# Performance work log

Measured on AMD Instinct MI355X. Metric: run time of the kernel, lower is better.

## Reference

```python
import jax, jax.numpy as jnp
import numpy as np

B, N, D = 4, 4096, 1024
STD = 1.0 / D

def setup_inputs() -> dict:
    key = jax.random.key(0)
    ks = jax.random.split(key, 6)
    return {
        "x_real": jax.random.normal(ks[0], (B, N, D), dtype=jnp.float32),
        "x_imag": jax.random.normal(ks[1], (B, N, D), dtype=jnp.float32),
        "w_query_real": jax.random.normal(ks[2], (D, D), dtype=jnp.float32) * STD,
        "w_query_imag": jax.random.normal(ks[3], (D, D), dtype=jnp.float32) * STD,
        "w_key": jax.random.normal(ks[4], (D, D), dtype=jnp.float32) * STD,
        "w_value": jax.random.normal(ks[5], (D, D), dtype=jnp.float32) * STD,
    }

def reference(x_real, x_imag, w_query_real, w_query_imag, w_key, w_value):
    # query gate: (x.real @ Wqr) * (x.imag @ Wqi)  -> [b, n, e]
    query = jnp.einsum('bnd,de->bne', x_real, w_query_real) * \
            jnp.einsum('bnd,de->bne', x_imag, w_query_imag)
    key = jnp.einsum('bnd,de->bne', x_real, w_key)      # [b, n, d]
    value = jnp.einsum('bnd,de->bne', x_imag, w_value)  # [b, n, e]
    # linear-attention style reduction over sequence dim n
    kv_attn = jnp.einsum('bnd,bne->bde', key, value)    # [b, d, e]
    # dropout with p=0.0 (eval / identity)
    bffn = jnp.einsum('bnd,bde->bne', query, kv_attn)   # [b, n, e]
    return bffn
```

## Files before the change

### kernel.cpp

```cpp
#include <hip/hip_runtime.h>
#include <stdint.h>

typedef unsigned short ushort_t;
typedef __attribute__((ext_vector_type(8))) short bf16x8;
typedef __attribute__((ext_vector_type(4))) float f32x4;

__device__ __forceinline__ ushort_t f2bf(float f) {
  union { float f; uint32_t u; } v; v.f = f;
  uint32_t u = v.u;
  u += 0x7FFFu + ((u >> 16) & 1u);
  return (ushort_t)(u >> 16);
}
__device__ __forceinline__ float bf2f(ushort_t h) {
  union { uint32_t u; float f; } v; v.u = ((uint32_t)h) << 16;
  return v.f;
}
__device__ __forceinline__ void gl2lds16(const void* g, void* l) {
  __builtin_amdgcn_global_load_lds(
      (__attribute__((address_space(1))) void*)(uintptr_t)g,
      (__attribute__((address_space(3))) void*)(uint32_t)(uintptr_t)l,
      16, 0, 0);
}


template <bool F32OUT>
__device__ __forceinline__ void gemm256x128(
    const ushort_t* __restrict__ A, int lda,
    const ushort_t* __restrict__ Bt, int ldb,
    int m0, int n0, int K, char* __restrict__ smem,
    f32x4 (&acc)[4][4]) {
  const int t = threadIdx.x;
  const int nt = K >> 5;
  const int rowS = t >> 2;
  const int kgS = (t & 3) ^ ((t >> 3) & 3);
  const ushort_t* a0 = A + (size_t)(m0 + rowS) * lda + kgS * 8;
  const ushort_t* a1 = a0 + (size_t)128 * lda;
  const ushort_t* b0 = Bt + (size_t)(n0 + rowS) * ldb + kgS * 8;
  const int d0 = t * 16;
  const int lane = t & 63, wid = t >> 6;
  const int wm = wid >> 1, wn = wid & 1;
  const int lr = lane & 15, lq = lane >> 4;
  const int o = lr * 64 + ((lq ^ ((lr >> 1) & 3)) << 4);
  const int aW = wm * 4096;
  const int bW = 16384 + wn * 4096;

#define STAGE(tt, buf) do { \
    char* s = smem + (buf); \
    gl2lds16(a0 + (tt) * 32, s + d0); \
    gl2lds16(a1 + (tt) * 32, s + 8192 + d0); \
    gl2lds16(b0 + (tt) * 32, s + 16384 + d0); \
  } while (0)

  bf16x8 aF[4], bF[4];
  STAGE(0, 0);
  for (int tt = 0; tt < nt; ++tt) {
    asm volatile("s_waitcnt vmcnt(0) lgkmcnt(0)\n\ts_barrier" ::: "memory");
    const int cb = (tt & 1) ? 24576 : 0;
    if (tt + 1 < nt) STAGE(tt + 1, (tt & 1) ? 0 : 24576);
    const char* base = smem + cb;
    #pragma unroll
    for (int mi = 0; mi < 4; ++mi)
      aF[mi] = *(const bf16x8*)(base + aW + mi * 1024 + o);
    #pragma unroll
    for (int ni = 0; ni < 4; ++ni)
      bF[ni] = *(const bf16x8*)(base + bW + ni * 1024 + o);
    __builtin_amdgcn_s_setprio(1);
    #pragma unroll
    for (int mi = 0; mi < 4; ++mi)
      #pragma unroll
      for (int ni = 0; ni < 4; ++ni)
        acc[mi][ni] = __builtin_amdgcn_mfma_f32_16x16x32_bf16(aF[mi], bF[ni], acc[mi][ni], 0, 0, 0);
    __builtin_amdgcn_s_setprio(0);
  }
#undef STAGE
}

__global__ __launch_bounds__(512, 2) void gq(
    const ushort_t* __restrict__ Xr, const ushort_t* __restrict__ Xi,
    const ushort_t* __restrict__ Wr, const ushort_t* __restrict__ Wi,
    ushort_t* __restrict__ Q) {
  extern __shared__ char smem[];
  const int bid = blockIdx.x;
  const int xcd = bid & 7, i = bid >> 3;
  const int m0 = (xcd * 8 + (i >> 3)) * 256;
  const int n0 = (i & 7) * 128;
  const int t = threadIdx.x;
  const int lane = t & 63, wid = t >> 6;
  const int wm = wid >> 1, wn = wid & 1;
  const int lr = lane & 15, lq = lane >> 4;

  const int rowS = t >> 2;
  const int kgS = (t & 3) ^ ((t >> 3) & 3);
  const ushort_t* ar0 = Xr + (size_t)(m0 + rowS) * 1024 + kgS * 8;
  const ushort_t* ar1 = ar0 + (size_t)128 * 1024;
  const ushort_t* ai0 = Xi + (size_t)(m0 + rowS) * 1024 + kgS * 8;
  const ushort_t* ai1 = ai0 + (size_t)128 * 1024;
  const ushort_t* br0 = Wr + (size_t)(n0 + rowS) * 1024 + kgS * 8;
  const ushort_t* bi0 = Wi + (size_t)(n0 + rowS) * 1024 + kgS * 8;
  const int d0 = t * 16;
  const int o = lr * 64 + ((lq ^ ((lr >> 1) & 3)) << 4);
  const int aW = wm * 4096;
  const int bW = wn * 4096;

#define STAGEQ(tt, buf) do { \
    char* s = smem + (buf); \
    gl2lds16(ar0 + (tt) * 32, s + d0); \
    gl2lds16(ar1 + (tt) * 32, s + 8192 + d0); \
    gl2lds16(ai0 + (tt) * 32, s + 16384 + d0); \
    gl2lds16(ai1 + (tt) * 32, s + 24576 + d0); \
    gl2lds16(br0 + (tt) * 32, s + 32768 + d0); \
    gl2lds16(bi0 + (tt) * 32, s + 40960 + d0); \
  } while (0)

  f32x4 accR[4][4] = {}, accI[4][4] = {};
  bf16x8 aR[4], aI[4], bR[4], bI[4];

  STAGEQ(0, 0);
  for (int tt = 0; tt < 32; ++tt) {
    asm volatile("s_waitcnt vmcnt(0) lgkmcnt(0)\n\ts_barrier" ::: "memory");
    const int cb = (tt & 1) ? 49152 : 0;
    if (tt + 1 < 32) STAGEQ(tt + 1, (tt & 1) ? 0 : 49152);
    const char* base = smem + cb;
    #pragma unroll
    for (int mi = 0; mi < 4; ++mi) {
      aR[mi] = *(const bf16x8*)(base + aW + mi * 1024 + o);
      aI[mi] = *(const bf16x8*)(base + 16384 + aW + mi * 1024 + o);
    }
    #pragma unroll
    for (int ni = 0; ni < 4; ++ni) {
      bR[ni] = *(const bf16x8*)(base + 32768 + bW + ni * 1024 + o);
      bI[ni] = *(const bf16x8*)(base + 40960 + bW + ni * 1024 + o);
    }
    __builtin_amdgcn_s_setprio(1);
    #pragma unroll
    for (int mi = 0; mi < 4; ++mi)
      #pragma unroll
      for (int ni = 0; ni < 4; ++ni) {
        accR[mi][ni] = __builtin_amdgcn_mfma_f32_16x16x32_bf16(aR[mi], bR[ni], accR[mi][ni], 0, 0, 0);
        accI[mi][ni] = __builtin_amdgcn_mfma_f32_16x16x32_bf16(aI[mi], bI[ni], accI[mi][ni], 0, 0, 0);
      }
    __builtin_amdgcn_s_setprio(0);
  }
#undef STAGEQ

  #pragma unroll
  for (int mi = 0; mi < 4; ++mi) {
    int rbase = m0 + wm * 64 + mi * 16 + lq * 4;
    #pragma unroll
    for (int ni = 0; ni < 4; ++ni) {
      int c = n0 + wn * 64 + ni * 16 + lr;
      #pragma unroll
      for (int r = 0; r < 4; ++r)
        Q[(size_t)(rbase + r) * 1024 + c] = f2bf(accR[mi][ni][r] * accI[mi][ni][r]);
    }
  }
}

__global__ __launch_bounds__(512, 4) void gpart(
    const ushort_t* __restrict__ XrT, const ushort_t* __restrict__ XiT,
    float* __restrict__ P) {
  extern __shared__ char smem[];
  const int bid = blockIdx.x;
  const int xcd = bid & 7, i = bid >> 3;
  const int z = xcd * 2 + (i >> 5);
  const int mn = i & 31;
  const int m0 = (mn >> 3) * 256, n0 = (mn & 7) * 128;
  const int b = z & 3, s = z >> 2;
  const ushort_t* A = XrT + ((size_t)b << 22) + s * 1024;
  const ushort_t* Bt = XiT + ((size_t)b << 22) + s * 1024;
  f32x4 acc[4][4] = {};
  gemm256x128<true>(A, 4096, Bt, 4096, m0, n0, 1024, smem, acc);

  const int t = threadIdx.x, lane = t & 63, wid = t >> 6;
  const int wm = wid >> 1, wn = wid & 1;
  const int lr = lane & 15, lq = lane >> 4;
  float* C = P + ((size_t)z << 20);
  #pragma unroll
  for (int mi = 0; mi < 4; ++mi) {
    int rbase = m0 + wm * 64 + mi * 16 + lq * 4;
    #pragma unroll
    for (int ni = 0; ni < 4; ++ni) {
      int c = n0 + wn * 64 + ni * 16 + lr;
      #pragma unroll
      for (int r = 0; r < 4; ++r)
        C[(size_t)(rbase + r) * 1024 + c] = acc[mi][ni][r];
    }
  }
}

__global__ __launch_bounds__(256) void g_reduce(const float* __restrict__ P,
                                                ushort_t* __restrict__ G) {
  size_t e4 = ((size_t)blockIdx.x * 256 + threadIdx.x) * 4;
  int b = (int)(e4 >> 20);
  size_t j = e4 & ((1u << 20) - 1);
  float s0 = 0.f, s1 = 0.f, s2 = 0.f, s3 = 0.f;
  #pragma unroll
  for (int sp = 0; sp < 4; ++sp) {
    float4 v = *(const float4*)(P + ((size_t)(sp * 4 + b) << 20) + j);
    s0 += v.x; s1 += v.y; s2 += v.z; s3 += v.w;
  }
  *(ushort4*)&G[e4] = make_ushort4(f2bf(s0), f2bf(s1), f2bf(s2), f2bf(s3));
}

__global__ __launch_bounds__(256, 4) void gemm1k(
    const ushort_t* __restrict__ Abase, int aStride,
    const ushort_t* __restrict__ Btbase, int btStride,
    ushort_t* __restrict__ Cbase) {
  extern __shared__ char smem[];
  const int bid = blockIdx.x;
  const int b = bid >> 6, mn = bid & 63;
  const int m0 = (mn >> 3) * 128, n0 = (mn & 7) * 128;
  const ushort_t* A = Abase + (size_t)b * (size_t)aStride;
  const ushort_t* Bt = Btbase + (size_t)b * (size_t)btStride;

  const int t = threadIdx.x;
  const int lane = t & 63, wid = t >> 6;
  const int wm = wid >> 1, wn = wid & 1;
  const int lr = lane & 15, lq = lane >> 4;
  const int rowS = t >> 2;
  const int kgS = (t & 3) ^ ((t >> 3) & 3);
  const ushort_t* a0 = A + (size_t)(m0 + rowS) * 1024 + kgS * 8;
  const ushort_t* a1 = a0 + (size_t)64 * 1024;
  const ushort_t* b0 = Bt + (size_t)(n0 + rowS) * 1024 + kgS * 8;
  const ushort_t* b1 = b0 + (size_t)64 * 1024;
  const int d0 = t * 16, d1 = 4096 + t * 16;
  const int o = lr * 64 + ((lq ^ ((lr >> 1) & 3)) << 4);
  const int aW = wm * 4096;
  const int bW = 8192 + wn * 4096;

#define STG1(tt, buf) do { \
    char* s = smem + (buf); \
    gl2lds16(a0 + (tt) * 32, s + d0); \
    gl2lds16(a1 + (tt) * 32, s + d1); \
    gl2lds16(b0 + (tt) * 32, s + 8192 + d0); \
    gl2lds16(b1 + (tt) * 32, s + 8192 + d1); \
  } while (0)

  f32x4 acc[4][4] = {};
  bf16x8 aF[4], bF[4];
  STG1(0, 0);
  for (int tt = 0; tt < 32; ++tt) {
    asm volatile("s_waitcnt vmcnt(0) lgkmcnt(0)\n\ts_barrier" ::: "memory");
    const int cb = (tt & 1) ? 16384 : 0;
    if (tt + 1 < 32) STG1(tt + 1, (tt & 1) ? 0 : 16384);
    const char* base = smem + cb;
    #pragma unroll
    for (int mi = 0; mi < 4; ++mi)
      aF[mi] = *(const bf16x8*)(base + aW + mi * 1024 + o);
    #pragma unroll
    for (int ni = 0; ni < 4; ++ni)
      bF[ni] = *(const bf16x8*)(base + bW + ni * 1024 + o);
    __builtin_amdgcn_s_setprio(1);
    #pragma unroll
    for (int mi = 0; mi < 4; ++mi)
      #pragma unroll
      for (int ni = 0; ni < 4; ++ni)
        acc[mi][ni] = __builtin_amdgcn_mfma_f32_16x16x32_bf16(aF[mi], bF[ni], acc[mi][ni], 0, 0, 0);
    __builtin_amdgcn_s_setprio(0);
  }
#undef STG1

  ushort_t* C = Cbase + ((size_t)b << 20);
  #pragma unroll
  for (int mi = 0; mi < 4; ++mi) {
    int rbase = m0 + wm * 64 + mi * 16 + lq * 4;
    #pragma unroll
    for (int ni = 0; ni < 4; ++ni) {
      int c = n0 + wn * 64 + ni * 16 + lr;
      #pragma unroll
      for (int r = 0; r < 4; ++r)
        C[(size_t)(rbase + r) * 1024 + c] = f2bf(acc[mi][ni][r]);
    }
  }
}

__global__ __launch_bounds__(512, 4) void fin8(
    const ushort_t* __restrict__ Q, const ushort_t* __restrict__ KVT,
    float* __restrict__ Out) {
  extern __shared__ char smem[];
  const int bid = blockIdx.x;
  const int xcd = bid & 7, i = bid >> 3;
  const int m0 = (xcd * 8 + (i >> 3)) * 256;
  const int n0 = (i & 7) * 128;
  const int b = m0 >> 12;
  f32x4 acc[4][4] = {};
  gemm256x128<true>(Q, 1024, KVT + ((size_t)b << 20), 1024, m0, n0, 1024, smem, acc);

  const int t = threadIdx.x, lane = t & 63, wid = t >> 6;
  const int wm = wid >> 1, wn = wid & 1;
  const int lr = lane & 15, lq = lane >> 4;
  #pragma unroll
  for (int mi = 0; mi < 4; ++mi) {
    int rbase = m0 + wm * 64 + mi * 16 + lq * 4;
    #pragma unroll
    for (int ni = 0; ni < 4; ++ni) {
      int c = n0 + wn * 64 + ni * 16 + lr;
      #pragma unroll
      for (int r = 0; r < 4; ++r)
        Out[(size_t)(rbase + r) * 1024 + c] = acc[mi][ni][r];
    }
  }
}

__global__ __launch_bounds__(256) void prep2(
    const float* __restrict__ xr, const float* __restrict__ xi,
    const float* w0, const float* w1, const float* w2, const float* w3,
    ushort_t* __restrict__ xrb, ushort_t* __restrict__ xib,
    ushort_t* __restrict__ xrT, ushort_t* __restrict__ xiT,
    ushort_t* o0, ushort_t* o1, ushort_t* o2, ushort_t* o3) {
  const int bid = blockIdx.x;
  const int t = threadIdx.x;
  __shared__ float tile[32][33];
  const int tx = t & 31, ty = t >> 5;
  if (bid < 4096) {
    const float* W; ushort_t* O;
    switch (bid >> 10) {
      case 0: W = w0; O = o0; break;
      case 1: W = w1; O = o1; break;
      case 2: W = w2; O = o2; break;
      default: W = w3; O = o3; break;
    }
    const int within = bid & 1023;
    const int bx = (within & 31) * 32, by = (within >> 5) * 32;
    #pragma unroll
    for (int k = 0; k < 32; k += 8)
      tile[ty + k][tx] = W[(size_t)(by + ty + k) * 1024 + bx + tx];
    __syncthreads();
    #pragma unroll
    for (int k = 0; k < 32; k += 8)
      O[(size_t)(bx + ty + k) * 1024 + by + tx] = f2bf(tile[tx][ty + k]);
  } else {
    const int xb = bid - 4096;
    const int tensor = xb >> 14;
    const int within = xb & 16383;
    const int by = (within >> 5) * 32;
    const int bx = (within & 31) * 32;
    const float* src = tensor ? xi : xr;
    ushort_t* dstS = tensor ? xib : xrb;
    ushort_t* dstT = tensor ? xiT : xrT;
    #pragma unroll
    for (int k = 0; k < 32; k += 8) {
      float v = src[(size_t)(by + ty + k) * 1024 + bx + tx];
      tile[ty + k][tx] = v;
      dstS[(size_t)(by + ty + k) * 1024 + bx + tx] = f2bf(v);
    }
    __syncthreads();
    const int b = by >> 12;
    const int nn = by & 4095;
    #pragma unroll
    for (int k = 0; k < 32; k += 8)
      dstT[((size_t)b << 22) + (size_t)(bx + ty + k) * 4096 + nn + tx] =
          f2bf(tile[tx][ty + k]);
  }
}

extern "C" void kernel_launch(void* const* d_in, const int* in_sizes, int n_in,
                              void* d_out, int out_size, void* d_ws, size_t ws_size,
                              hipStream_t stream) {
  const float* xr  = (const float*)d_in[0];
  const float* xi  = (const float*)d_in[1];
  const float* wqr = (const float*)d_in[2];
  const float* wqi = (const float*)d_in[3];
  const float* wk  = (const float*)d_in[4];
  const float* wv  = (const float*)d_in[5];

  char* ws = (char*)d_ws;
  const size_t MB = 1024ull * 1024ull;
  ushort_t* WtQR = (ushort_t*)(ws + 0 * MB);
  ushort_t* WtQI = (ushort_t*)(ws + 2 * MB);
  ushort_t* WtK  = (ushort_t*)(ws + 4 * MB);
  ushort_t* WtV  = (ushort_t*)(ws + 6 * MB);
  ushort_t* XrT  = (ushort_t*)(ws + 8 * MB);
  ushort_t* XiT  = (ushort_t*)(ws + 40 * MB);
  ushort_t* Q    = (ushort_t*)(ws + 72 * MB);
  ushort_t* G    = (ushort_t*)(ws + 104 * MB);
  ushort_t* H    = (ushort_t*)(ws + 8 * MB);
  ushort_t* KVT  = (ushort_t*)(ws + 16 * MB);
  ushort_t* Xrb  = (ushort_t*)d_out;
  ushort_t* Xib  = (ushort_t*)((char*)d_out + 32 * MB);
  float*    Pf   = (float*)d_out;

  static bool inited = false;
  if (!inited) {
    inited = true;
    hipFuncSetAttribute((const void*)&gq,     hipFuncAttributeMaxDynamicSharedMemorySize, 98304);
    hipFuncSetAttribute((const void*)&gpart,  hipFuncAttributeMaxDynamicSharedMemorySize, 49152);
    hipFuncSetAttribute((const void*)&gemm1k, hipFuncAttributeMaxDynamicSharedMemorySize, 32768);
    hipFuncSetAttribute((const void*)&fin8,   hipFuncAttributeMaxDynamicSharedMemorySize, 49152);
  }

  prep2<<<36864, 256, 0, stream>>>(xr, xi, wqr, wqi, wk, wv,
                                   Xrb, Xib, XrT, XiT, WtQR, WtQI, WtK, WtV);
  gq<<<512, 512, 98304, stream>>>(Xrb, Xib, WtQR, WtQI, Q);
  gpart<<<512, 512, 49152, stream>>>(XrT, XiT, Pf);
  g_reduce<<<4096, 256, 0, stream>>>(Pf, G);
  gemm1k<<<256, 256, 32768, stream>>>(WtV, 0, G, 1 << 20, H);
  gemm1k<<<256, 256, 32768, stream>>>(H, 1 << 20, WtK, 0, KVT);
  fin8<<<512, 512, 49152, stream>>>(Q, KVT, (float*)d_out);
}
```

Before: 438.9 us.

## Halve gq LDS, store split-K partials as bf16, retile gemm1k and prep transpose

The gq kernel now stages the real and imaginary operand halves in alternating 24KB buffers instead of double-buffering both at once. That halves its LDS footprint, at the cost of an extra barrier per K step. gpart writes its split-K partials as bf16 instead of fp32, cutting the traffic into and out of g_reduce but adding rounding error before the reduction. gemm1k moves to 128-thread blocks with 128x64 tiles across 512 blocks. The prep transpose uses 64x64 tiles with float4 loads and 16-byte bf16 stores.

Result: faster. 424.0 us (-3.4%).

```diff
diff --git a/kernel.cpp b/kernel.cpp
--- a/kernel.cpp
+++ b/kernel.cpp
@@ -23,7 +23,6 @@
 }
 
 
-template <bool F32OUT>
 __device__ __forceinline__ void gemm256x128(
     const ushort_t* __restrict__ A, int lda,
     const ushort_t* __restrict__ Bt, int ldb,
@@ -100,48 +99,49 @@
   const int d0 = t * 16;
   const int o = lr * 64 + ((lq ^ ((lr >> 1) & 3)) << 4);
   const int aW = wm * 4096;
-  const int bW = wn * 4096;
-
-#define STAGEQ(tt, buf) do { \
+  const int bW = 16384 + wn * 4096;
+
+#define STG3(p0, p1, pb, ks, buf) do { \
     char* s = smem + (buf); \
-    gl2lds16(ar0 + (tt) * 32, s + d0); \
-    gl2lds16(ar1 + (tt) * 32, s + 8192 + d0); \
-    gl2lds16(ai0 + (tt) * 32, s + 16384 + d0); \
-    gl2lds16(ai1 + (tt) * 32, s + 24576 + d0); \
-    gl2lds16(br0 + (tt) * 32, s + 32768 + d0); \
-    gl2lds16(bi0 + (tt) * 32, s + 40960 + d0); \
+    gl2lds16(p0 + (ks) * 32, s + d0); \
+    gl2lds16(p1 + (ks) * 32, s + 8192 + d0); \
+    gl2lds16(pb + (ks) * 32, s + 16384 + d0); \
   } while (0)
+#define RDFRAG(buf) do { \
+    const char* base = smem + (buf); \
+    _Pragma("unroll") \
+    for (int mi = 0; mi < 4; ++mi) aF[mi] = *(const bf16x8*)(base + aW + mi * 1024 + o); \
+    _Pragma("unroll") \
+    for (int ni = 0; ni < 4; ++ni) bF[ni] = *(const bf16x8*)(base + bW + ni * 1024 + o); \
+  } while (0)
+#define MM(ACC) \
+    __builtin_amdgcn_s_setprio(1); \
+    _Pragma("unroll") \
+    for (int mi = 0; mi < 4; ++mi) \
+      _Pragma("unroll") \
+      for (int ni = 0; ni < 4; ++ni) \
+        ACC[mi][ni] = __builtin_amdgcn_mfma_f32_16x16x32_bf16(aF[mi], bF[ni], ACC[mi][ni], 0, 0, 0); \
+    __builtin_amdgcn_s_setprio(0);
+#define BND() asm volatile("s_waitcnt vmcnt(0) lgkmcnt(0)\n\ts_barrier" ::: "memory")
 
   f32x4 accR[4][4] = {}, accI[4][4] = {};
-  bf16x8 aR[4], aI[4], bR[4], bI[4];
-
-  STAGEQ(0, 0);
-  for (int tt = 0; tt < 32; ++tt) {
-    asm volatile("s_waitcnt vmcnt(0) lgkmcnt(0)\n\ts_barrier" ::: "memory");
-    const int cb = (tt & 1) ? 49152 : 0;
-    if (tt + 1 < 32) STAGEQ(tt + 1, (tt & 1) ? 0 : 49152);
-    const char* base = smem + cb;
-    #pragma unroll
-    for (int mi = 0; mi < 4; ++mi) {
-      aR[mi] = *(const bf16x8*)(base + aW + mi * 1024 + o);
-      aI[mi] = *(const bf16x8*)(base + 16384 + aW + mi * 1024 + o);
-    }
-    #pragma unroll
-    for (int ni = 0; ni < 4; ++ni) {
-      bR[ni] = *(const bf16x8*)(base + 32768 + bW + ni * 1024 + o);
-      bI[ni] = *(const bf16x8*)(base + 40960 + bW + ni * 1024 + o);
-    }
-    __builtin_amdgcn_s_setprio(1);
-    #pragma unroll
-    for (int mi = 0; mi < 4; ++mi)
-      #pragma unroll
-      for (int ni = 0; ni < 4; ++ni) {
-        accR[mi][ni] = __builtin_amdgcn_mfma_f32_16x16x32_bf16(aR[mi], bR[ni], accR[mi][ni], 0, 0, 0);
-        accI[mi][ni] = __builtin_amdgcn_mfma_f32_16x16x32_bf16(aI[mi], bI[ni], accI[mi][ni], 0, 0, 0);
-      }
-    __builtin_amdgcn_s_setprio(0);
-  }
-#undef STAGEQ
+  bf16x8 aF[4], bF[4];
+
+  STG3(ar0, ar1, br0, 0, 0);
+  for (int ks = 0; ks < 32; ++ks) {
+    BND();
+    STG3(ai0, ai1, bi0, ks, 24576);
+    RDFRAG(0);
+    MM(accR)
+    BND();
+    if (ks + 1 < 32) STG3(ar0, ar1, br0, ks + 1, 0);
+    RDFRAG(24576);
+    MM(accI)
+  }
+#undef STG3
+#undef RDFRAG
+#undef MM
+#undef BND
 
   #pragma unroll
   for (int mi = 0; mi < 4; ++mi) {
@@ -158,7 +158,7 @@
 
 __global__ __launch_bounds__(512, 4) void gpart(
     const ushort_t* __restrict__ XrT, const ushort_t* __restrict__ XiT,
-    float* __restrict__ P) {
+    ushort_t* __restrict__ P) {
   extern __shared__ char smem[];
   const int bid = blockIdx.x;
   const int xcd = bid & 7, i = bid >> 3;
@@ -169,12 +169,12 @@
   const ushort_t* A = XrT + ((size_t)b << 22) + s * 1024;
   const ushort_t* Bt = XiT + ((size_t)b << 22) + s * 1024;
   f32x4 acc[4][4] = {};
-  gemm256x128<true>(A, 4096, Bt, 4096, m0, n0, 1024, smem, acc);
+  gemm256x128(A, 4096, Bt, 4096, m0, n0, 1024, smem, acc);
 
   const int t = threadIdx.x, lane = t & 63, wid = t >> 6;
   const int wm = wid >> 1, wn = wid & 1;
   const int lr = lane & 15, lq = lane >> 4;
-  float* C = P + ((size_t)z << 20);
+  ushort_t* C = P + ((size_t)z << 20);
   #pragma unroll
   for (int mi = 0; mi < 4; ++mi) {
     int rbase = m0 + wm * 64 + mi * 16 + lq * 4;
@@ -183,12 +183,12 @@
       int c = n0 + wn * 64 + ni * 16 + lr;
       #pragma unroll
       for (int r = 0; r < 4; ++r)
-        C[(size_t)(rbase + r) * 1024 + c] = acc[mi][ni][r];
-    }
-  }
-}
-
-__global__ __launch_bounds__(256) void g_reduce(const float* __restrict__ P,
+        C[(size_t)(rbase + r) * 1024 + c] = f2bf(acc[mi][ni][r]);
+    }
+  }
+}
+
+__global__ __launch_bounds__(256) void g_reduce(const ushort_t* __restrict__ P,
                                                 ushort_t* __restrict__ G) {
   size_t e4 = ((size_t)blockIdx.x * 256 + threadIdx.x) * 4;
   int b = (int)(e4 >> 20);
@@ -196,44 +196,57 @@
   float s0 = 0.f, s1 = 0.f, s2 = 0.f, s3 = 0.f;
   #pragma unroll
   for (int sp = 0; sp < 4; ++sp) {
-    float4 v = *(const float4*)(P + ((size_t)(sp * 4 + b) << 20) + j);
-    s0 += v.x; s1 += v.y; s2 += v.z; s3 += v.w;
+    ushort4 v = *(const ushort4*)(P + ((size_t)(sp * 4 + b) << 20) + j);
+    s0 += bf2f(v.x); s1 += bf2f(v.y); s2 += bf2f(v.z); s3 += bf2f(v.w);
   }
   *(ushort4*)&G[e4] = make_ushort4(f2bf(s0), f2bf(s1), f2bf(s2), f2bf(s3));
 }
 
-__global__ __launch_bounds__(256, 4) void gemm1k(
+__global__ __launch_bounds__(128, 4) void gemm1k(
     const ushort_t* __restrict__ Abase, int aStride,
     const ushort_t* __restrict__ Btbase, int btStride,
     ushort_t* __restrict__ Cbase) {
   extern __shared__ char smem[];
   const int bid = blockIdx.x;
-  const int b = bid >> 6, mn = bid & 63;
-  const int m0 = (mn >> 3) * 128, n0 = (mn & 7) * 128;
+  const int b = bid >> 7, mn = bid & 127;
+  const int m0 = (mn >> 4) * 128, n0 = (mn & 15) * 64;
   const ushort_t* A = Abase + (size_t)b * (size_t)aStride;
   const ushort_t* Bt = Btbase + (size_t)b * (size_t)btStride;
 
   const int t = threadIdx.x;
   const int lane = t & 63, wid = t >> 6;
-  const int wm = wid >> 1, wn = wid & 1;
   const int lr = lane & 15, lq = lane >> 4;
-  const int rowS = t >> 2;
-  const int kgS = (t & 3) ^ ((t >> 3) & 3);
-  const ushort_t* a0 = A + (size_t)(m0 + rowS) * 1024 + kgS * 8;
-  const ushort_t* a1 = a0 + (size_t)64 * 1024;
-  const ushort_t* b0 = Bt + (size_t)(n0 + rowS) * 1024 + kgS * 8;
-  const ushort_t* b1 = b0 + (size_t)64 * 1024;
-  const int d0 = t * 16, d1 = 4096 + t * 16;
+
+  const ushort_t* pa[4];
+  const ushort_t* pb[2];
+  int dA[4], dB[2];
+  #pragma unroll
+  for (int p = 0; p < 4; ++p) {
+    int ch = p * 128 + t;
+    int row = ch >> 2;
+    int kg = (ch & 3) ^ ((row >> 1) & 3);
+    pa[p] = A + (size_t)(m0 + row) * 1024 + kg * 8;
+    dA[p] = ch * 16;
+  }
+  #pragma unroll
+  for (int p = 0; p < 2; ++p) {
+    int ch = p * 128 + t;
+    int row = ch >> 2;
+    int kg = (ch & 3) ^ ((row >> 1) & 3);
+    pb[p] = Bt + (size_t)(n0 + row) * 1024 + kg * 8;
+    dB[p] = 8192 + ch * 16;
+  }
   const int o = lr * 64 + ((lq ^ ((lr >> 1) & 3)) << 4);
-  const int aW = wm * 4096;
-  const int bW = 8192 + wn * 4096;
+  const int aW = wid * 4096;
 
 #define STG1(tt, buf) do { \
     char* s = smem + (buf); \
-    gl2lds16(a0 + (tt) * 32, s + d0); \
-    gl2lds16(a1 + (tt) * 32, s + d1); \
-    gl2lds16(b0 + (tt) * 32, s + 8192 + d0); \
-    gl2lds16(b1 + (tt) * 32, s + 8192 + d1); \
+    gl2lds16(pa[0] + (tt) * 32, s + dA[0]); \
+    gl2lds16(pa[1] + (tt) * 32, s + dA[1]); \
+    gl2lds16(pa[2] + (tt) * 32, s + dA[2]); \
+    gl2lds16(pa[3] + (tt) * 32, s + dA[3]); \
+    gl2lds16(pb[0] + (tt) * 32, s + dB[0]); \
+    gl2lds16(pb[1] + (tt) * 32, s + dB[1]); \
   } while (0)
 
   f32x4 acc[4][4] = {};
@@ -241,15 +254,15 @@
   STG1(0, 0);
   for (int tt = 0; tt < 32; ++tt) {
     asm volatile("s_waitcnt vmcnt(0) lgkmcnt(0)\n\ts_barrier" ::: "memory");
-    const int cb = (tt & 1) ? 16384 : 0;
-    if (tt + 1 < 32) STG1(tt + 1, (tt & 1) ? 0 : 16384);
+    const int cb = (tt & 1) ? 12288 : 0;
+    if (tt + 1 < 32) STG1(tt + 1, (tt & 1) ? 0 : 12288);
     const char* base = smem + cb;
     #pragma unroll
     for (int mi = 0; mi < 4; ++mi)
       aF[mi] = *(const bf16x8*)(base + aW + mi * 1024 + o);
     #pragma unroll
     for (int ni = 0; ni < 4; ++ni)
-      bF[ni] = *(const bf16x8*)(base + bW + ni * 1024 + o);
+      bF[ni] = *(const bf16x8*)(base + 8192 + ni * 1024 + o);
     __builtin_amdgcn_s_setprio(1);
     #pragma unroll
     for (int mi = 0; mi < 4; ++mi)
@@ -263,10 +276,10 @@
   ushort_t* C = Cbase + ((size_t)b << 20);
   #pragma unroll
   for (int mi = 0; mi < 4; ++mi) {
-    int rbase = m0 + wm * 64 + mi * 16 + lq * 4;
+    int rbase = m0 + wid * 64 + mi * 16 + lq * 4;
     #pragma unroll
     for (int ni = 0; ni < 4; ++ni) {
-      int c = n0 + wn * 64 + ni * 16 + lr;
+      int c = n0 + ni * 16 + lr;
       #pragma unroll
       for (int r = 0; r < 4; ++r)
         C[(size_t)(rbase + r) * 1024 + c] = f2bf(acc[mi][ni][r]);
@@ -284,7 +297,7 @@
   const int n0 = (i & 7) * 128;
   const int b = m0 >> 12;
   f32x4 acc[4][4] = {};
-  gemm256x128<true>(Q, 1024, KVT + ((size_t)b << 20), 1024, m0, n0, 1024, smem, acc);
+  gemm256x128(Q, 1024, KVT + ((size_t)b << 20), 1024, m0, n0, 1024, smem, acc);
 
   const int t = threadIdx.x, lane = t & 63, wid = t >> 6;
   const int wm = wid >> 1, wn = wid & 1;
@@ -310,9 +323,9 @@
     ushort_t* o0, ushort_t* o1, ushort_t* o2, ushort_t* o3) {
   const int bid = blockIdx.x;
   const int t = threadIdx.x;
-  __shared__ float tile[32][33];
-  const int tx = t & 31, ty = t >> 5;
   if (bid < 4096) {
+    __shared__ float tile[32][33];
+    const int tx = t & 31, ty = t >> 5;
     const float* W; ushort_t* O;
     switch (bid >> 10) {
       case 0: W = w0; O = o0; break;
@@ -330,27 +343,45 @@
     for (int k = 0; k < 32; k += 8)
       O[(size_t)(bx + ty + k) * 1024 + by + tx] = f2bf(tile[tx][ty + k]);
   } else {
+    __shared__ float tx64[64][65];
     const int xb = bid - 4096;
-    const int tensor = xb >> 14;
-    const int within = xb & 16383;
-    const int by = (within >> 5) * 32;
-    const int bx = (within & 31) * 32;
+    const int tensor = xb >> 12;
+    const int within = xb & 4095;
+    const int n0 = (within >> 4) * 64;
+    const int d0g = (within & 15) * 64;
     const float* src = tensor ? xi : xr;
     ushort_t* dstS = tensor ? xib : xrb;
     ushort_t* dstT = tensor ? xiT : xrT;
-    #pragma unroll
-    for (int k = 0; k < 32; k += 8) {
-      float v = src[(size_t)(by + ty + k) * 1024 + bx + tx];
-      tile[ty + k][tx] = v;
-      dstS[(size_t)(by + ty + k) * 1024 + bx + tx] = f2bf(v);
+    const int r = t >> 2;
+    const int c4 = (t & 3) * 4;
+    #pragma unroll
+    for (int p = 0; p < 4; ++p) {
+      float4 v = *(const float4*)&src[(size_t)(n0 + r) * 1024 + d0g + c4 + p * 16];
+      tx64[r][c4 + p * 16 + 0] = v.x;
+      tx64[r][c4 + p * 16 + 1] = v.y;
+      tx64[r][c4 + p * 16 + 2] = v.z;
+      tx64[r][c4 + p * 16 + 3] = v.w;
     }
     __syncthreads();
-    const int b = by >> 12;
-    const int nn = by & 4095;
-    #pragma unroll
-    for (int k = 0; k < 32; k += 8)
-      dstT[((size_t)b << 22) + (size_t)(bx + ty + k) * 4096 + nn + tx] =
-          f2bf(tile[tx][ty + k]);
+    {
+      const int c0 = (t & 3) * 16;
+      ushort_t tmp[16];
+      #pragma unroll
+      for (int j = 0; j < 16; ++j) tmp[j] = f2bf(tx64[r][c0 + j]);
+      ushort_t* p = &dstS[(size_t)(n0 + r) * 1024 + d0g + c0];
+      *(bf16x8*)&p[0] = *(const bf16x8*)&tmp[0];
+      *(bf16x8*)&p[8] = *(const bf16x8*)&tmp[8];
+    }
+    {
+      const int nb = (t & 3) * 16;
+      ushort_t tmp[16];
+      #pragma unroll
+      for (int j = 0; j < 16; ++j) tmp[j] = f2bf(tx64[nb + j][r]);
+      const int b = n0 >> 12, nn = n0 & 4095;
+      ushort_t* p = &dstT[((size_t)b << 22) + (size_t)(d0g + r) * 4096 + nn + nb];
+      *(bf16x8*)&p[0] = *(const bf16x8*)&tmp[0];
+      *(bf16x8*)&p[8] = *(const bf16x8*)&tmp[8];
+    }
   }
 }
 
@@ -378,23 +409,23 @@
   ushort_t* KVT  = (ushort_t*)(ws + 16 * MB);
   ushort_t* Xrb  = (ushort_t*)d_out;
   ushort_t* Xib  = (ushort_t*)((char*)d_out + 32 * MB);
-  float*    Pf   = (float*)d_out;
+  ushort_t* Pb   = (ushort_t*)d_out;
 
   static bool inited = false;
   if (!inited) {
     inited = true;
-    hipFuncSetAttribute((const void*)&gq,     hipFuncAttributeMaxDynamicSharedMemorySize, 98304);
+    hipFuncSetAttribute((const void*)&gq,     hipFuncAttributeMaxDynamicSharedMemorySize, 49152);
     hipFuncSetAttribute((const void*)&gpart,  hipFuncAttributeMaxDynamicSharedMemorySize, 49152);
-    hipFuncSetAttribute((const void*)&gemm1k, hipFuncAttributeMaxDynamicSharedMemorySize, 32768);
+    hipFuncSetAttribute((const void*)&gemm1k, hipFuncAttributeMaxDynamicSharedMemorySize, 24576);
     hipFuncSetAttribute((const void*)&fin8,   hipFuncAttributeMaxDynamicSharedMemorySize, 49152);
   }
 
-  prep2<<<36864, 256, 0, stream>>>(xr, xi, wqr, wqi, wk, wv,
+  prep2<<<12288, 256, 0, stream>>>(xr, xi, wqr, wqi, wk, wv,
                                    Xrb, Xib, XrT, XiT, WtQR, WtQI, WtK, WtV);
-  gq<<<512, 512, 98304, stream>>>(Xrb, Xib, WtQR, WtQI, Q);
-  gpart<<<512, 512, 49152, stream>>>(XrT, XiT, Pf);
-  g_reduce<<<4096, 256, 0, stream>>>(Pf, G);
-  gemm1k<<<256, 256, 32768, stream>>>(WtV, 0, G, 1 << 20, H);
-  gemm1k<<<256, 256, 32768, stream>>>(H, 1 << 20, WtK, 0, KVT);
+  gq<<<512, 512, 49152, stream>>>(Xrb, Xib, WtQR, WtQI, Q);
+  gpart<<<512, 512, 49152, stream>>>(XrT, XiT, Pb);
+  g_reduce<<<4096, 256, 0, stream>>>(Pb, G);
+  gemm1k<<<512, 128, 24576, stream>>>(WtV, 0, G, 1 << 20, H);
+  gemm1k<<<512, 128, 24576, stream>>>(H, 1 << 20, WtK, 0, KVT);
   fin8<<<512, 512, 49152, stream>>>(Q, KVT, (float*)d_out);
 }
```
